# Kernel tuning notes

Hardware: AMD Instinct MI355X
Metric: run time of the kernel (lower is better)

Reference implementation:

```python
import jax, jax.numpy as jnp
import numpy as np


def _haar_filters():
    # pywt 'haar': dec_lo = [s, s], dec_hi = [-s, s], s = 1/sqrt(2)
    s = np.float32(1.0 / np.sqrt(2.0))
    lo = np.array([s, s], dtype=np.float32)
    hi = np.array([-s, s], dtype=np.float32)
    # torch conv2d is cross-correlation; filter_2d = outer(row, col)
    # order matches module output concat: LL, LH, HL, HH
    f = np.stack([
        np.outer(lo, lo),  # LL
        np.outer(lo, hi),  # LH
        np.outer(hi, lo),  # HL
        np.outer(hi, hi),  # HH
    ]).astype(np.float32)  # (4, 2, 2)
    return jnp.asarray(f)


def setup_inputs() -> dict:
    key = jax.random.key(0)
    x = jax.random.normal(key, (8, 32, 512, 512), dtype=jnp.float32)
    return {"x": x, "filters": _haar_filters()}


def reference(x, filters):
    """Haar DWT2D: (B,C,H,W) -> (B,4C,H//2+1,W//2+1).

    Matches torch: pad to even dims (zeros), reflect-pad by 1,
    2x2 cross-correlation with stride 2 per subband, channel-concat
    [LL | LH | HL | HH].
    """
    b, c, h, w = x.shape
    pad_h = (2 - h % 2) % 2
    pad_w = (2 - w % 2) % 2
    if pad_h or pad_w:  # static shapes -> jit-safe Python branch
        x = jnp.pad(x, ((0, 0), (0, 0), (0, pad_h), (0, pad_w)))
    xp = jnp.pad(x, ((0, 0), (0, 0), (1, 1), (1, 1)), mode="reflect")
    # Stride-2 2x2 windows: tap (di,dj) of window (i,j) is xp[2i+di, 2j+dj].
    # xp has H+2 rows -> H//2 + 1 window rows (same for cols).
    x00 = xp[:, :, 0::2, 0::2]
    x01 = xp[:, :, 0::2, 1::2]
    x10 = xp[:, :, 1::2, 0::2]
    x11 = xp[:, :, 1::2, 1::2]
    win = jnp.stack([x00, x01, x10, x11], axis=-1)  # (B,C,h2,w2,4)
    f = filters.reshape(4, 4)                        # (subband, tap)
    out = jnp.einsum("bchwt,kt->bkchw", win, f)      # (B,4,C,h2,w2)
    b_, k_, c_, h2, w2 = out.shape
    return out.reshape(b_, k_ * c_, h2, w2)


if __name__ == "__main__":
    inp = setup_inputs()
    y = reference(**inp)
    print(y.shape, y.dtype)
```

## Files before the change

kernel.cpp:

```cpp
#include <hip/hip_runtime.h>


constexpr int H_IN  = 512;
constexpr int W_IN  = 512;
constexpr int H_OUT = 257;
constexpr int W_OUT = 257;
constexpr long long PLANE_OUT = (long long)H_OUT * W_OUT;
constexpr long long PLANE_IN  = (long long)H_IN * W_IN;

__global__ __launch_bounds__(256)
void dwt2d_haar_rows(const float* __restrict__ x,
                     const float* __restrict__ filt,
                     float* __restrict__ out) {
    const int i  = blockIdx.x;
    const int bc = blockIdx.y;
    const int t  = threadIdx.x;

    __shared__ float row0[W_IN];
    __shared__ float row1[W_IN];

    int r0 = 2 * i - 1; if (r0 < 0)     r0 = 1;
    int r1 = 2 * i;     if (r1 >= H_IN) r1 = H_IN - 2;

    const float* xp = x + (long long)bc * PLANE_IN;

    {
        const int half = t >> 7;
        const int lane = (t & 127) << 2;
        const float* src = xp + (long long)(half ? r1 : r0) * W_IN + lane;
        float4 v = *reinterpret_cast<const float4*>(src);
        float* dst = (half ? row1 : row0) + lane;
        dst[0] = v.x; dst[1] = v.y; dst[2] = v.z; dst[3] = v.w;
    }
    __syncthreads();

    float F[16];
#pragma unroll
    for (int k = 0; k < 16; ++k) F[k] = filt[k];

    const int bb = bc >> 5;
    const int cc = bc & 31;
    const long long obase = (long long)(bb * 128 + cc) * PLANE_OUT
                          + (long long)i * W_OUT;

    {
        int c0 = 2 * t - 1; if (c0 < 0) c0 = 1;
        int c1 = 2 * t;
        float a = row0[c0], b = row0[c1];
        float c = row1[c0], d = row1[c1];
#pragma unroll
        for (int k = 0; k < 4; ++k) {
            float v = F[4*k+0] * a + F[4*k+1] * b + F[4*k+2] * c + F[4*k+3] * d;
            __builtin_nontemporal_store(v, &out[obase + (long long)(k * 32) * PLANE_OUT + t]);
        }
    }
    if (t == 0) {
        float a = row0[511], b = row0[510];
        float c = row1[511], d = row1[510];
#pragma unroll
        for (int k = 0; k < 4; ++k) {
            float v = F[4*k+0] * a + F[4*k+1] * b + F[4*k+2] * c + F[4*k+3] * d;
            __builtin_nontemporal_store(v, &out[obase + (long long)(k * 32) * PLANE_OUT + 256]);
        }
    }
}

extern "C" void kernel_launch(void* const* d_in, const int* in_sizes, int n_in,
                              void* d_out, int out_size, void* d_ws, size_t ws_size,
                              hipStream_t stream) {
    const float* x    = (const float*)d_in[0];
    const float* filt = (const float*)d_in[1];
    float*       out  = (float*)d_out;

    dim3 grid(H_OUT, 256);
    dwt2d_haar_rows<<<grid, 256, 0, stream>>>(x, filt, out);
}
```

Measured before the change: 94.52 us.

## Process 16 output rows per block with double-buffered register prefetch

```diff
diff --git a/kernel.cpp b/kernel.cpp
--- a/kernel.cpp
+++ b/kernel.cpp
@@ -5,63 +5,75 @@
 constexpr int W_IN  = 512;
 constexpr int H_OUT = 257;
 constexpr int W_OUT = 257;
+constexpr int NROWS = 16;
 constexpr long long PLANE_OUT = (long long)H_OUT * W_OUT;
 constexpr long long PLANE_IN  = (long long)H_IN * W_IN;
 
 __global__ __launch_bounds__(256)
-void dwt2d_haar_rows(const float* __restrict__ x,
+void dwt2d_haar_pipe(const float* __restrict__ x,
                      const float* __restrict__ filt,
                      float* __restrict__ out) {
-    const int i  = blockIdx.x;
+    const int ib = blockIdx.x * NROWS;
     const int bc = blockIdx.y;
     const int t  = threadIdx.x;
 
-    __shared__ float row0[W_IN];
-    __shared__ float row1[W_IN];
+    __shared__ float buf[2][2][W_IN];
 
-    int r0 = 2 * i - 1; if (r0 < 0)     r0 = 1;
-    int r1 = 2 * i;     if (r1 >= H_IN) r1 = H_IN - 2;
+    const float* xp   = x + (long long)bc * PLANE_IN;
+    const int    half = t >> 7;
+    const int    lane = (t & 127) << 2;
 
-    const float* xp = x + (long long)bc * PLANE_IN;
-
-    {
-        const int half = t >> 7;
-        const int lane = (t & 127) << 2;
-        const float* src = xp + (long long)(half ? r1 : r0) * W_IN + lane;
-        float4 v = *reinterpret_cast<const float4*>(src);
-        float* dst = (half ? row1 : row0) + lane;
-        dst[0] = v.x; dst[1] = v.y; dst[2] = v.z; dst[3] = v.w;
-    }
-    __syncthreads();
+    auto load_pair = [&](int i) -> float4 {
+        int r0 = 2 * i - 1; if (r0 < 0)     r0 = 1;
+        int r1 = 2 * i;     if (r1 >= H_IN) r1 = H_IN - 2;
+        const int r = half ? r1 : r0;
+        return *reinterpret_cast<const float4*>(xp + r * W_IN + lane);
+    };
 
     float F[16];
 #pragma unroll
     for (int k = 0; k < 16; ++k) F[k] = filt[k];
 
-    const int bb = bc >> 5;
-    const int cc = bc & 31;
-    const long long obase = (long long)(bb * 128 + cc) * PLANE_OUT
-                          + (long long)i * W_OUT;
+    const int bb = bc >> 5, cc = bc & 31;
+    const long long plane_base = (long long)(bb * 128 + cc) * PLANE_OUT;
 
-    {
+    const int nvalid = (H_OUT - ib < NROWS) ? (H_OUT - ib) : NROWS;
+
+    float4 v = load_pair(ib);
+    int cur = 0;
+    for (int it = 0; it < nvalid; ++it) {
+        const int i = ib + it;
+
+        float* dst = &buf[cur][half][lane];
+        dst[0] = v.x; dst[1] = v.y; dst[2] = v.z; dst[3] = v.w;
+
+        if (it + 1 < nvalid) v = load_pair(i + 1);
+
+        __syncthreads();
+
+        const float* r0p = buf[cur][0];
+        const float* r1p = buf[cur][1];
         int c0 = 2 * t - 1; if (c0 < 0) c0 = 1;
         int c1 = 2 * t;
-        float a = row0[c0], b = row0[c1];
-        float c = row1[c0], d = row1[c1];
+        float a = r0p[c0], b = r0p[c1];
+        float c = r1p[c0], d = r1p[c1];
+
+        const long long obase = plane_base + (long long)i * W_OUT;
 #pragma unroll
         for (int k = 0; k < 4; ++k) {
-            float v = F[4*k+0] * a + F[4*k+1] * b + F[4*k+2] * c + F[4*k+3] * d;
-            __builtin_nontemporal_store(v, &out[obase + (long long)(k * 32) * PLANE_OUT + t]);
+            float vv = F[4*k+0] * a + F[4*k+1] * b + F[4*k+2] * c + F[4*k+3] * d;
+            __builtin_nontemporal_store(vv, &out[obase + (long long)(k * 32) * PLANE_OUT + t]);
         }
-    }
-    if (t == 0) {
-        float a = row0[511], b = row0[510];
-        float c = row1[511], d = row1[510];
+        if (t == 0) {
+            float a2 = r0p[511], b2 = r0p[510];
+            float c2 = r1p[511], d2 = r1p[510];
 #pragma unroll
-        for (int k = 0; k < 4; ++k) {
-            float v = F[4*k+0] * a + F[4*k+1] * b + F[4*k+2] * c + F[4*k+3] * d;
-            __builtin_nontemporal_store(v, &out[obase + (long long)(k * 32) * PLANE_OUT + 256]);
+            for (int k = 0; k < 4; ++k) {
+                float vv = F[4*k+0] * a2 + F[4*k+1] * b2 + F[4*k+2] * c2 + F[4*k+3] * d2;
+                __builtin_nontemporal_store(vv, &out[obase + (long long)(k * 32) * PLANE_OUT + 256]);
+            }
         }
+        cur ^= 1;
     }
 }
 
@@ -72,6 +84,6 @@
     const float* filt = (const float*)d_in[1];
     float*       out  = (float*)d_out;
 
-    dim3 grid(H_OUT, 256);
-    dwt2d_haar_rows<<<grid, 256, 0, stream>>>(x, filt, out);
+    dim3 grid((H_OUT + NROWS - 1) / NROWS, 256);
+    dwt2d_haar_pipe<<<grid, 256, 0, stream>>>(x, filt, out);
 }
```

Result: slower. 111.8 us (+18.3%).
